# Optimization experiments

Hardware: AMD Instinct MI355X
Metric: run time of the kernel (lower is better)

## Reference

```python
import jax, jax.numpy as jnp
import numpy as np

B, T, C, H = 2, 2048, 2048, 16  # batch, seq_len, dim, num_heads
D = C // H  # head_dim = 128
ROPE_BASE = 10000.0


def apply_rope(x, pos):
    # x: [B, T, H, D]; adjacent-pair rotation (torchtune convention)
    d = x.shape[-1]
    inv_freq = 1.0 / (ROPE_BASE ** (jnp.arange(0, d, 2, dtype=jnp.float32) / d))  # [D/2]
    freqs = pos.astype(jnp.float32)[:, None] * inv_freq[None, :]                 # [T, D/2]
    cos = jnp.cos(freqs)[None, :, None, :]
    sin = jnp.sin(freqs)[None, :, None, :]
    x1 = x[..., 0::2]
    x2 = x[..., 1::2]
    out = jnp.stack([x1 * cos - x2 * sin, x2 * cos + x1 * sin], axis=-1)  # [B,T,H,D/2,2]
    return out.reshape(x.shape)


def setup_inputs() -> dict:
    key = jax.random.key(0)
    k1, k2, k3 = jax.random.split(key, 3)
    x = jax.random.normal(k1, (B, T, C), dtype=jnp.float32)
    # 0.02 init scale keeps attention logits in a sane range
    W_qkv = jax.random.normal(k2, (C, 3 * C), dtype=jnp.float32) * 0.02
    W_out = jax.random.normal(k3, (C, C), dtype=jnp.float32) * 0.02
    return {"x": x, "W_qkv": W_qkv, "W_out": W_out}


def reference(x, W_qkv, W_out):
    b, t, c = x.shape
    h, d = H, c // H
    # fused QKV projection
    qkv = (x @ W_qkv).reshape(b, t, 3, h, d)
    q, k, v = qkv[:, :, 0], qkv[:, :, 1], qkv[:, :, 2]  # [B,T,H,D] each
    pos = jnp.arange(t)  # cache_pos = 0 (prefill)
    q = apply_rope(q, pos)
    k = apply_rope(k, pos)
    scale = 1.0 / np.sqrt(d).astype(np.float32)
    scores = jnp.einsum('bqhd,bkhd->bhqk', q, k) * scale  # [B,H,T,T]
    causal = jnp.tril(jnp.ones((t, t), dtype=bool))
    scores = jnp.where(causal[None, None], scores, -jnp.inf)
    probs = jax.nn.softmax(scores, axis=-1)
    o = jnp.einsum('bhqk,bkhd->bqhd', probs, v).reshape(b, t, c)
    return o @ W_out
```

## Files before the change

kernel.cpp:

```cpp
#include <hip/hip_runtime.h>
#include <stdint.h>

#define TSEQ 2048

typedef __bf16 bf16x8 __attribute__((ext_vector_type(8)));
typedef float f32x4 __attribute__((ext_vector_type(4)));

typedef const __attribute__((address_space(1))) unsigned int* gas_u32;
typedef __attribute__((address_space(3))) unsigned int* las_u32;

__device__ __forceinline__ f32x4 mfma16(bf16x8 a, bf16x8 b, f32x4 c) {
  return __builtin_amdgcn_mfma_f32_16x16x32_bf16(a, b, c, 0, 0, 0);
}

__device__ __forceinline__ unsigned short f2b(float f) {
  unsigned int u = __float_as_uint(f);
  u += 0x7fffu + ((u >> 16) & 1u);
  return (unsigned short)(u >> 16);
}

__device__ __forceinline__ void gload_lds16(const unsigned short* g, unsigned short* l) {
  __builtin_amdgcn_global_load_lds((gas_u32)(const void*)g, (las_u32)(void*)l, 16, 0, 0);
}

__global__ __launch_bounds__(256) void cast_bf16_kernel(const float* __restrict__ src,
                                                        unsigned short* __restrict__ dst) {
  size_t i = ((size_t)blockIdx.x * 256 + threadIdx.x) * 4;
  float4 v = *(const float4*)(src + i);
  ushort4 o;
  o.x = f2b(v.x); o.y = f2b(v.y); o.z = f2b(v.z); o.w = f2b(v.w);
  *(ushort4*)(dst + i) = o;
}

__device__ __forceinline__ void transpose_tile(const float* __restrict__ src,
                                               unsigned short* __restrict__ dst,
                                               int R, int Cc, int cb, int rb) {
  __shared__ float tile[64][65];
  int t = threadIdx.x;
  int tr = t >> 4;
  int tc = (t & 15) * 4;
#pragma unroll
  for (int i = 0; i < 4; i++) {
    int r = tr + 16 * i;
    float4 v = *(const float4*)(src + (size_t)(rb + r) * Cc + cb + tc);
    tile[r][tc + 0] = v.x; tile[r][tc + 1] = v.y;
    tile[r][tc + 2] = v.z; tile[r][tc + 3] = v.w;
  }
  __syncthreads();
#pragma unroll
  for (int i = 0; i < 4; i++) {
    int r2 = tr + 16 * i;
    ushort4 o;
    o.x = f2b(tile[tc + 0][r2]);
    o.y = f2b(tile[tc + 1][r2]);
    o.z = f2b(tile[tc + 2][r2]);
    o.w = f2b(tile[tc + 3][r2]);
    *(ushort4*)(dst + (size_t)(cb + r2) * R + rb + tc) = o;
  }
}

__global__ __launch_bounds__(256) void transpose_cast2_kernel(const float* __restrict__ srcA,
                                                              unsigned short* __restrict__ dstA,
                                                              const float* __restrict__ srcB,
                                                              unsigned short* __restrict__ dstB) {
  int bx = blockIdx.x, rb = blockIdx.y * 64;
  if (bx < 96) transpose_tile(srcA, dstA, 2048, 6144, bx * 64, rb);
  else         transpose_tile(srcB, dstB, 2048, 2048, (bx - 96) * 64, rb);
}

__device__ __forceinline__ void gemm_core_256(const unsigned short* __restrict__ A,
                                              const unsigned short* __restrict__ Bt,
                                              int K, int bm, int bn,
                                              unsigned short* sm,
                                              f32x4 (&acc)[4][8]) {
  const int t = threadIdx.x;
  const int lane = t & 63, w = t >> 6;
  const int wloc = w & 3;
  const int wm = (wloc >> 1) * 64;
  const int wn = (wloc & 1) * 128;
  const int ks = w >> 2;
  const int quad = lane >> 4, l16 = lane & 15;
  const int rsw = l16 & 7;
  const int ch = ((ks * 4 + quad) ^ rsw) * 8;

  const int srow = t >> 3;
  const int gch = (t & 7) ^ (srow & 7);
  const unsigned short* pA = A + (size_t)(bm + srow) * K + gch * 8;
  const unsigned short* pB = Bt + (size_t)(bn + srow) * K + gch * 8;
  const size_t K64 = (size_t)64 * K;

  auto stageA = [&](int k0, unsigned short* dstSlot) {
    gload_lds16(pA + k0, dstSlot + t * 8);
    gload_lds16(pA + K64 + k0, dstSlot + (t + 512) * 8);
  };
  auto stageB01 = [&](int k0, unsigned short* dstSlot) {
    unsigned short* tB = dstSlot + 8192;
    gload_lds16(pB + k0, tB + t * 8);
    gload_lds16(pB + K64 + k0, tB + (t + 512) * 8);
  };
  auto stageB23 = [&](int k0, unsigned short* dstSlot) {
    unsigned short* tB = dstSlot + 8192;
    gload_lds16(pB + 2 * K64 + k0, tB + (t + 1024) * 8);
    gload_lds16(pB + 3 * K64 + k0, tB + (t + 1536) * 8);
  };

  stageA(0, sm);          stageB01(0, sm);          stageB23(0, sm);
  stageA(64, sm + 24576); stageB01(64, sm + 24576); stageB23(64, sm + 24576);

  const int nIter = K >> 6;
  int scur = 0, sstg = 2;

#pragma unroll 1
  for (int it = 0; it < nIter; it++) {
    if (it + 1 < nIter)
      asm volatile("s_waitcnt vmcnt(6) lgkmcnt(0)" ::: "memory");
    else
      asm volatile("s_waitcnt vmcnt(0) lgkmcnt(0)" ::: "memory");
    __builtin_amdgcn_s_barrier();
    asm volatile("" ::: "memory");

    const unsigned short* sA = sm + scur * 24576;
    const unsigned short* sB = sA + 8192;
    unsigned short* tgt = sm + sstg * 24576;
    const bool doStage = (it + 2 < nIter);
    const int k2 = (it + 2) << 6;

    bf16x8 aF[4], bF[8];

    auto mm = [&](int jb) {
      __builtin_amdgcn_s_setprio(1);
#pragma unroll
      for (int i = 0; i < 4; i++)
#pragma unroll
        for (int j2 = 0; j2 < 2; j2++)
          acc[i][jb + j2] = mfma16(aF[i], bF[jb + j2], acc[i][jb + j2]);
      __builtin_amdgcn_s_setprio(0);
    };

#pragma unroll
    for (int i = 0; i < 4; i++)
      aF[i] = *(const bf16x8*)(sA + (wm + i * 16 + l16) * 64 + ch);
#pragma unroll
    for (int j = 0; j < 2; j++)
      bF[j] = *(const bf16x8*)(sB + (wn + j * 16 + l16) * 64 + ch);
    if (doStage) stageA(k2, tgt);
    mm(0);
#pragma unroll
    for (int j = 2; j < 4; j++)
      bF[j] = *(const bf16x8*)(sB + (wn + j * 16 + l16) * 64 + ch);
    if (doStage) stageB01(k2, tgt);
    mm(2);
#pragma unroll
    for (int j = 4; j < 6; j++)
      bF[j] = *(const bf16x8*)(sB + (wn + j * 16 + l16) * 64 + ch);
    if (doStage) stageB23(k2, tgt);
    mm(4);
#pragma unroll
    for (int j = 6; j < 8; j++)
      bF[j] = *(const bf16x8*)(sB + (wn + j * 16 + l16) * 64 + ch);
    mm(6);

    scur = (scur == 2) ? 0 : scur + 1;
    sstg = (sstg == 2) ? 0 : sstg + 1;
  }
  __syncthreads();

  {
    float* mbuf = (float*)sm;
    float* wb = mbuf + w * 4096;
    const int lane4 = lane * 4;
    if (w < 4) {
#pragma unroll
      for (int i2 = 0; i2 < 2; i2++)
#pragma unroll
        for (int j = 0; j < 8; j++)
          *(f32x4*)(wb + (i2 * 8 + j) * 256 + lane4) = acc[2 + i2][j];
    } else {
#pragma unroll
      for (int i2 = 0; i2 < 2; i2++)
#pragma unroll
        for (int j = 0; j < 8; j++)
          *(f32x4*)(wb + (i2 * 8 + j) * 256 + lane4) = acc[i2][j];
    }
    __syncthreads();
    const float* pb = mbuf + (w ^ 4) * 4096;
    if (w < 4) {
#pragma unroll
      for (int i2 = 0; i2 < 2; i2++)
#pragma unroll
        for (int j = 0; j < 8; j++)
          acc[i2][j] += *(const f32x4*)(pb + (i2 * 8 + j) * 256 + lane4);
    } else {
#pragma unroll
      for (int i2 = 0; i2 < 2; i2++)
#pragma unroll
        for (int j = 0; j < 8; j++)
          acc[i2][j] = acc[2 + i2][j] + *(const f32x4*)(pb + (i2 * 8 + j) * 256 + lane4);
    }
  }
}

__global__ __launch_bounds__(512, 2) void gemm_qkv_rope(const unsigned short* __restrict__ Xb,
                                                        const unsigned short* __restrict__ Wqt,
                                                        unsigned short* __restrict__ Qd,
                                                        unsigned short* __restrict__ Kd,
                                                        unsigned short* __restrict__ Vtd) {
  __shared__ unsigned short smem[73728];
  f32x4 acc[4][8];
  const f32x4 z = {0.f, 0.f, 0.f, 0.f};
#pragma unroll
  for (int i = 0; i < 4; i++)
#pragma unroll
    for (int j = 0; j < 8; j++) acc[i][j] = z;

  const int bm = blockIdx.y * 128;
  const int bn = blockIdx.x * 256;
  gemm_core_256(Xb, Wqt, 2048, bm, bn, smem, acc);

  const int c0 = blockIdx.x * 2;
  const int s = c0 >> 4;
  const int hA = c0 & 15, hB = (c0 + 1) & 15;
  const int t = threadIdx.x, lane = t & 63, w = t >> 6;
  const int wloc = w & 3;
  const int wm = (wloc >> 1) * 64, wn = (wloc & 1) * 128;
  const int rowbase = wm + (w >> 2) * 32;
  const int quad = lane >> 4, l16 = lane & 15;
  const int bq = bm >> 11;
  const int tpos0 = bm & (TSEQ - 1);

  __syncthreads();
  unsigned short* sC = smem;

  if (s < 2) {
    const float scl = (s == 0) ? 0.08838834764831845f : 1.0f;
#pragma unroll
    for (int j = 0; j < 8; j++) {
      int d = wn + j * 16 + l16;
      int dh = d & 127;
      float invf = __expf(-(float)(dh >> 1) * 0.14391157f);
#pragma unroll
      for (int i = 0; i < 2; i++) {
#pragma unroll
        for (int r = 0; r < 4; r++) {
          int row = rowbase + i * 16 + quad * 4 + r;
          float ang = (float)(tpos0 + row) * invf;
          float sn, cs;
          __sincosf(ang, &sn, &cs);
          float v = acc[i][j][r];
          float p = __shfl_xor(v, 1, 64);
          float outv = (d & 1) ? (v * cs + p * sn) : (v * cs - p * sn);
          sC[row * 264 + d] = f2b(outv * scl);
        }
      }
    }
    __syncthreads();
    unsigned short* dst = (s == 0) ? Qd : Kd;
#pragma unroll
    for (int it = 0; it < 8; it++) {
      int u = t + 512 * it;
      int row = u >> 5, cc = u & 31;
      int hl = cc >> 4;
      size_t gb = ((size_t)(bq * 16 + (hl ? hB : hA)) * TSEQ + tpos0 + row) * 128 + (cc & 15) * 8;
      *(uint4*)(dst + gb) = *(const uint4*)(sC + row * 264 + cc * 8);
    }
  } else {
#pragma unroll
    for (int j = 0; j < 8; j++) {
      int d = wn + j * 16 + l16;
#pragma unroll
      for (int i = 0; i < 2; i++)
#pragma unroll
        for (int r = 0; r < 4; r++) {
          int col = rowbase + i * 16 + quad * 4 + r;
          sC[d * 136 + col] = f2b(acc[i][j][r]);
        }
    }
    __syncthreads();
#pragma unroll
    for (int it = 0; it < 8; it++) {
      int u = t + 512 * it;
      int dd = u >> 4, cc = u & 15;
      int hl = dd >> 7, dl = dd & 127;
      size_t gb = ((size_t)(bq * 16 + (hl ? hB : hA)) * 128 + dl) * TSEQ + tpos0 + cc * 8;
      *(uint4*)(Vtd + gb) = *(const uint4*)(sC + dd * 136 + cc * 8);
    }
  }
}

__global__ __launch_bounds__(256, 2) void attn_kernel(const unsigned short* __restrict__ Q,
                                                      const unsigned short* __restrict__ Kmat,
                                                      const unsigned short* __restrict__ Vt,
                                                      unsigned short* __restrict__ Ob) {
  __shared__ unsigned short smem[37376];
  const int pair = blockIdx.x, bh = blockIdx.y;
  const int qA = pair, qB = 31 - pair;
  const int t = threadIdx.x, lane = t & 63, w = t >> 6, quad = lane >> 4, l16 = lane & 15;
  const size_t base = (size_t)bh * TSEQ * 128;
  const unsigned short* Qp = Q + base;
  const unsigned short* Kp = Kmat + base;
  const unsigned short* Vp = Vt + base;
  unsigned short* myP = smem + 32768 + w * 1152;

  bf16x8 aqA[4], aqB[4];
  {
    int qrA = qA * 64 + w * 16 + l16;
    int qrB = qB * 64 + w * 16 + l16;
#pragma unroll
    for (int kk = 0; kk < 4; kk++) {
      aqA[kk] = *(const bf16x8*)(Qp + (size_t)qrA * 128 + kk * 32 + quad * 8);
      aqB[kk] = *(const bf16x8*)(Qp + (size_t)qrB * 128 + kk * 32 + quad * 8);
    }
  }
  const f32x4 z = {0.f, 0.f, 0.f, 0.f};
  f32x4 oA[8], oB[8];
  float mA[4], lA[4], mB[4], lB[4];
#pragma unroll
  for (int dt = 0; dt < 8; dt++) { oA[dt] = z; oB[dt] = z; }
#pragma unroll
  for (int r = 0; r < 4; r++) { mA[r] = -1e30f; lA[r] = 0.f; mB[r] = -1e30f; lB[r] = 0.f; }

  auto load_tiles = [&](int kb, int buf) {
    unsigned short* bK = smem + buf * 16384;
    unsigned short* bV = bK + 8192;
    const unsigned short* Kt = Kp + (size_t)kb * 64 * 128;
#pragma unroll
    for (int i2 = 0; i2 < 4; i2++) {
      int idx = t + 256 * i2;
      int r = idx >> 4, cS = idx & 15;
      int c = cS ^ (r & 7);
      gload_lds16(Kt + r * 128 + c * 8, bK + idx * 8);
    }
#pragma unroll
    for (int i2 = 0; i2 < 4; i2++) {
      int idx = t + 256 * i2;
      int r = idx >> 3, cS = idx & 7;
      int c = cS ^ (r & 7);
      gload_lds16(Vp + (size_t)r * TSEQ + kb * 64 + c * 8, bV + idx * 8);
    }
  };

  auto process = [&](bf16x8 (&aq)[4], f32x4 (&o)[8], float (&mst)[4], float (&lst)[4],
                     int qb, int kb, const unsigned short* bK, const unsigned short* bV) {
    f32x4 S[4];
#pragma unroll
    for (int nt = 0; nt < 4; nt++) {
      f32x4 sacc = z;
#pragma unroll
      for (int kk = 0; kk < 4; kk++) {
        const unsigned short* p =
            bK + (nt * 16 + l16) * 128 + (((kk * 4 + quad) ^ (l16 & 7)) * 8);
        sacc = mfma16(aq[kk], *(const bf16x8*)p, sacc);
      }
      S[nt] = sacc;
    }
    if (kb == qb) {
      int qg = qb * 64 + w * 16 + quad * 4;
#pragma unroll
      for (int nt = 0; nt < 4; nt++) {
        int key = kb * 64 + nt * 16 + l16;
#pragma unroll
        for (int r = 0; r < 4; r++)
          if (key > qg + r) S[nt][r] = -1e30f;
      }
    }
    float alpha[4];
#pragma unroll
    for (int r = 0; r < 4; r++) {
      float mx = fmaxf(fmaxf(S[0][r], S[1][r]), fmaxf(S[2][r], S[3][r]));
      mx = fmaxf(mx, __shfl_xor(mx, 1, 64));
      mx = fmaxf(mx, __shfl_xor(mx, 2, 64));
      mx = fmaxf(mx, __shfl_xor(mx, 4, 64));
      mx = fmaxf(mx, __shfl_xor(mx, 8, 64));
      float mnew = fmaxf(mst[r], mx);
      alpha[r] = __expf(mst[r] - mnew);
      mst[r] = mnew;
    }
    float rs[4] = {0.f, 0.f, 0.f, 0.f};
#pragma unroll
    for (int nt = 0; nt < 4; nt++)
#pragma unroll
      for (int r = 0; r < 4; r++) {
        float p = __expf(S[nt][r] - mst[r]);
        S[nt][r] = p;
        rs[r] += p;
      }
#pragma unroll
    for (int r = 0; r < 4; r++) {
      float s4 = rs[r];
      s4 += __shfl_xor(s4, 1, 64);
      s4 += __shfl_xor(s4, 2, 64);
      s4 += __shfl_xor(s4, 4, 64);
      s4 += __shfl_xor(s4, 8, 64);
      lst[r] = lst[r] * alpha[r] + s4;
#pragma unroll
      for (int nt = 0; nt < 4; nt++)
        myP[(quad * 4 + r) * 72 + nt * 16 + l16] = f2b(S[nt][r]);
    }
#pragma unroll
    for (int dt = 0; dt < 8; dt++) {
      f32x4 ov = o[dt];
      ov[0] *= alpha[0]; ov[1] *= alpha[1]; ov[2] *= alpha[2]; ov[3] *= alpha[3];
      o[dt] = ov;
    }
#pragma unroll
    for (int kk = 0; kk < 2; kk++) {
      bf16x8 ap = *(const bf16x8*)(myP + l16 * 72 + kk * 32 + quad * 8);
#pragma unroll
      for (int dt = 0; dt < 8; dt++) {
        const unsigned short* p =
            bV + (dt * 16 + l16) * 64 + (((kk * 4 + quad) ^ (l16 & 7)) * 8);
        o[dt] = mfma16(ap, *(const bf16x8*)p, o[dt]);
      }
    }
  };

  load_tiles(0, 0);
#pragma unroll 1
  for (int kb = 0; kb <= qB; kb++) {
    __syncthreads();
    if (kb < qB) load_tiles(kb + 1, (kb + 1) & 1);
    const unsigned short* bK = smem + (kb & 1) * 16384;
    const unsigned short* bV = bK + 8192;
    process(aqB, oB, mB, lB, qB, kb, bK, bV);
    if (kb <= qA) process(aqA, oA, mA, lA, qA, kb, bK, bV);
  }

  __syncthreads();
  unsigned short* sOA = smem;
  unsigned short* sOB = smem + 8704;
#pragma unroll
  for (int dt = 0; dt < 8; dt++)
#pragma unroll
    for (int r = 0; r < 4; r++) {
      int row = w * 16 + quad * 4 + r;
      sOA[row * 136 + dt * 16 + l16] = f2b(oA[dt][r] / lA[r]);
      sOB[row * 136 + dt * 16 + l16] = f2b(oB[dt][r] / lB[r]);
    }
  __syncthreads();
  const int b = bh >> 4, h = bh & 15;
#pragma unroll
  for (int it = 0; it < 4; it++) {
    int c = t + 256 * it;
    int row = c >> 4, off = (c & 15) * 8;
    uint4 va = *(const uint4*)(sOA + row * 136 + off);
    *(uint4*)(Ob + (size_t)(b * TSEQ + qA * 64 + row) * 2048 + h * 128 + off) = va;
    uint4 vb = *(const uint4*)(sOB + row * 136 + off);
    *(uint4*)(Ob + (size_t)(b * TSEQ + qB * 64 + row) * 2048 + h * 128 + off) = vb;
  }
}

__global__ __launch_bounds__(512, 2) void gemm_out_kernel(const unsigned short* __restrict__ Ob,
                                                          const unsigned short* __restrict__ Wot,
                                                          float* __restrict__ Cout) {
  __shared__ unsigned short smem[73728];
  f32x4 acc[4][8];
  const f32x4 z = {0.f, 0.f, 0.f, 0.f};
#pragma unroll
  for (int i = 0; i < 4; i++)
#pragma unroll
    for (int j = 0; j < 8; j++) acc[i][j] = z;

  const int bm = blockIdx.y * 128, bn = blockIdx.x * 256;
  gemm_core_256(Ob, Wot, 2048, bm, bn, smem, acc);

  const int t = threadIdx.x, lane = t & 63, w = t >> 6;
  const int wloc = w & 3;
  const int wm = (wloc >> 1) * 64, wn = (wloc & 1) * 128;
  const int rowbase = wm + (w >> 2) * 32;
  const int quad = lane >> 4, l16 = lane & 15;
#pragma unroll
  for (int i = 0; i < 2; i++)
#pragma unroll
    for (int j = 0; j < 8; j++)
#pragma unroll
      for (int r = 0; r < 4; r++) {
        int row = bm + rowbase + i * 16 + quad * 4 + r;
        int col = bn + wn + j * 16 + l16;
        Cout[(size_t)row * 2048 + col] = acc[i][j][r];
      }
}

extern "C" void kernel_launch(void* const* d_in, const int* in_sizes, int n_in,
                              void* d_out, int out_size, void* d_ws, size_t ws_size,
                              hipStream_t stream) {
  (void)in_sizes; (void)n_in; (void)out_size; (void)ws_size;
  const float* x = (const float*)d_in[0];
  const float* Wqkv = (const float*)d_in[1];
  const float* Wout = (const float*)d_in[2];
  float* out = (float*)d_out;
  char* ws = (char*)d_ws;

  unsigned short* Xb  = (unsigned short*)(ws);
  unsigned short* Wqt = (unsigned short*)(ws + 16777216);
  unsigned short* Wot = (unsigned short*)(ws + 41943040);
  unsigned short* Qd  = (unsigned short*)(ws + 50331648);
  unsigned short* Kd  = (unsigned short*)(ws + 67108864);
  unsigned short* Vtd = (unsigned short*)(ws + 83886080);
  unsigned short* Obf = (unsigned short*)(ws + 100663296);

  cast_bf16_kernel<<<8192, 256, 0, stream>>>(x, Xb);
  transpose_cast2_kernel<<<dim3(128, 32), 256, 0, stream>>>(Wqkv, Wqt, Wout, Wot);
  gemm_qkv_rope<<<dim3(24, 32), 512, 0, stream>>>(Xb, Wqt, Qd, Kd, Vtd);
  attn_kernel<<<dim3(16, 32), 256, 0, stream>>>(Qd, Kd, Vtd, Obf);
  gemm_out_kernel<<<dim3(8, 32), 512, 0, stream>>>(Obf, Wot, out);
}
```

Measured before the change: 379.7 us.

## Share K/V LDS fragments across paired query tiles and merge prologue kernels

```diff
diff --git a/kernel.cpp b/kernel.cpp
--- a/kernel.cpp
+++ b/kernel.cpp
@@ -21,15 +21,6 @@
 
 __device__ __forceinline__ void gload_lds16(const unsigned short* g, unsigned short* l) {
   __builtin_amdgcn_global_load_lds((gas_u32)(const void*)g, (las_u32)(void*)l, 16, 0, 0);
-}
-
-__global__ __launch_bounds__(256) void cast_bf16_kernel(const float* __restrict__ src,
-                                                        unsigned short* __restrict__ dst) {
-  size_t i = ((size_t)blockIdx.x * 256 + threadIdx.x) * 4;
-  float4 v = *(const float4*)(src + i);
-  ushort4 o;
-  o.x = f2b(v.x); o.y = f2b(v.y); o.z = f2b(v.z); o.w = f2b(v.w);
-  *(ushort4*)(dst + i) = o;
 }
 
 __device__ __forceinline__ void transpose_tile(const float* __restrict__ src,
@@ -59,13 +50,25 @@
   }
 }
 
-__global__ __launch_bounds__(256) void transpose_cast2_kernel(const float* __restrict__ srcA,
-                                                              unsigned short* __restrict__ dstA,
-                                                              const float* __restrict__ srcB,
-                                                              unsigned short* __restrict__ dstB) {
-  int bx = blockIdx.x, rb = blockIdx.y * 64;
-  if (bx < 96) transpose_tile(srcA, dstA, 2048, 6144, bx * 64, rb);
-  else         transpose_tile(srcB, dstB, 2048, 2048, (bx - 96) * 64, rb);
+__global__ __launch_bounds__(256) void prologue_kernel(const float* __restrict__ x,
+                                                       unsigned short* __restrict__ Xb,
+                                                       const float* __restrict__ Wqkv,
+                                                       unsigned short* __restrict__ Wqt,
+                                                       const float* __restrict__ Wout,
+                                                       unsigned short* __restrict__ Wot) {
+  int n = blockIdx.x;
+  if (n < 8192) {
+    size_t i = ((size_t)n * 256 + threadIdx.x) * 4;
+    float4 v = *(const float4*)(x + i);
+    ushort4 o;
+    o.x = f2b(v.x); o.y = f2b(v.y); o.z = f2b(v.z); o.w = f2b(v.w);
+    *(ushort4*)(Xb + i) = o;
+  } else {
+    int m = n - 8192;
+    int bxx = m & 127, rb = (m >> 7) * 64;
+    if (bxx < 96) transpose_tile(Wqkv, Wqt, 2048, 6144, bxx * 64, rb);
+    else          transpose_tile(Wout, Wot, 2048, 2048, (bxx - 96) * 64, rb);
+  }
 }
 
 __device__ __forceinline__ void gemm_core_256(const unsigned short* __restrict__ A,
@@ -339,30 +342,8 @@
     }
   };
 
-  auto process = [&](bf16x8 (&aq)[4], f32x4 (&o)[8], float (&mst)[4], float (&lst)[4],
-                     int qb, int kb, const unsigned short* bK, const unsigned short* bV) {
-    f32x4 S[4];
-#pragma unroll
-    for (int nt = 0; nt < 4; nt++) {
-      f32x4 sacc = z;
-#pragma unroll
-      for (int kk = 0; kk < 4; kk++) {
-        const unsigned short* p =
-            bK + (nt * 16 + l16) * 128 + (((kk * 4 + quad) ^ (l16 & 7)) * 8);
-        sacc = mfma16(aq[kk], *(const bf16x8*)p, sacc);
-      }
-      S[nt] = sacc;
-    }
-    if (kb == qb) {
-      int qg = qb * 64 + w * 16 + quad * 4;
-#pragma unroll
-      for (int nt = 0; nt < 4; nt++) {
-        int key = kb * 64 + nt * 16 + l16;
-#pragma unroll
-        for (int r = 0; r < 4; r++)
-          if (key > qg + r) S[nt][r] = -1e30f;
-      }
-    }
+  auto softmax_pv = [&](f32x4 (&S)[4], f32x4 (&o)[8], float (&mst)[4], float (&lst)[4],
+                        const unsigned short* bV, bool loadV, bf16x8 (&vr)[16]) {
     float alpha[4];
 #pragma unroll
     for (int r = 0; r < 4; r++) {
@@ -407,10 +388,22 @@
       bf16x8 ap = *(const bf16x8*)(myP + l16 * 72 + kk * 32 + quad * 8);
 #pragma unroll
       for (int dt = 0; dt < 8; dt++) {
-        const unsigned short* p =
-            bV + (dt * 16 + l16) * 64 + (((kk * 4 + quad) ^ (l16 & 7)) * 8);
-        o[dt] = mfma16(ap, *(const bf16x8*)p, o[dt]);
+        if (loadV)
+          vr[kk * 8 + dt] = *(const bf16x8*)(bV + (dt * 16 + l16) * 64 +
+                                             (((kk * 4 + quad) ^ (l16 & 7)) * 8));
+        o[dt] = mfma16(ap, vr[kk * 8 + dt], o[dt]);
       }
+    }
+  };
+
+  auto mask_tile = [&](f32x4 (&S)[4], int qb, int kb) {
+    int qg = qb * 64 + w * 16 + quad * 4;
+#pragma unroll
+    for (int nt = 0; nt < 4; nt++) {
+      int key = kb * 64 + nt * 16 + l16;
+#pragma unroll
+      for (int r = 0; r < 4; r++)
+        if (key > qg + r) S[nt][r] = -1e30f;
     }
   };
 
@@ -421,8 +414,42 @@
     if (kb < qB) load_tiles(kb + 1, (kb + 1) & 1);
     const unsigned short* bK = smem + (kb & 1) * 16384;
     const unsigned short* bV = bK + 8192;
-    process(aqB, oB, mB, lB, qB, kb, bK, bV);
-    if (kb <= qA) process(aqA, oA, mA, lA, qA, kb, bK, bV);
+
+    if (kb <= qA) {
+      f32x4 SB[4], SA[4];
+#pragma unroll
+      for (int nt = 0; nt < 4; nt++) {
+        f32x4 sb = z, sa = z;
+#pragma unroll
+        for (int kk = 0; kk < 4; kk++) {
+          bf16x8 kf = *(const bf16x8*)(bK + (nt * 16 + l16) * 128 +
+                                       (((kk * 4 + quad) ^ (l16 & 7)) * 8));
+          sb = mfma16(aqB[kk], kf, sb);
+          sa = mfma16(aqA[kk], kf, sa);
+        }
+        SB[nt] = sb; SA[nt] = sa;
+      }
+      if (kb == qA) mask_tile(SA, qA, kb);
+      bf16x8 vr[16];
+      softmax_pv(SB, oB, mB, lB, bV, true, vr);
+      softmax_pv(SA, oA, mA, lA, bV, false, vr);
+    } else {
+      f32x4 SB[4];
+#pragma unroll
+      for (int nt = 0; nt < 4; nt++) {
+        f32x4 sb = z;
+#pragma unroll
+        for (int kk = 0; kk < 4; kk++) {
+          bf16x8 kf = *(const bf16x8*)(bK + (nt * 16 + l16) * 128 +
+                                       (((kk * 4 + quad) ^ (l16 & 7)) * 8));
+          sb = mfma16(aqB[kk], kf, sb);
+        }
+        SB[nt] = sb;
+      }
+      if (kb == qB) mask_tile(SB, qB, kb);
+      bf16x8 vr[16];
+      softmax_pv(SB, oB, mB, lB, bV, true, vr);
+    }
   }
 
   __syncthreads();
@@ -498,8 +525,7 @@
   unsigned short* Vtd = (unsigned short*)(ws + 83886080);
   unsigned short* Obf = (unsigned short*)(ws + 100663296);
 
-  cast_bf16_kernel<<<8192, 256, 0, stream>>>(x, Xb);
-  transpose_cast2_kernel<<<dim3(128, 32), 256, 0, stream>>>(Wqkv, Wqt, Wout, Wot);
+  prologue_kernel<<<12288, 256, 0, stream>>>(x, Xb, Wqkv, Wqt, Wout, Wot);
   gemm_qkv_rope<<<dim3(24, 32), 512, 0, stream>>>(Xb, Wqt, Qd, Kd, Vtd);
   attn_kernel<<<dim3(16, 32), 256, 0, stream>>>(Qd, Kd, Vtd, Obf);
   gemm_out_kernel<<<dim3(8, 32), 512, 0, stream>>>(Obf, Wot, out);
```

Result: slower. 439.2 us (+15.7%).

## Merge prologue cast/transpose kernels and add intra-iteration barriers to GEMM core

Applied to the files above, without the earlier changes.

```diff
diff --git a/kernel.cpp b/kernel.cpp
--- a/kernel.cpp
+++ b/kernel.cpp
@@ -21,15 +21,6 @@
 
 __device__ __forceinline__ void gload_lds16(const unsigned short* g, unsigned short* l) {
   __builtin_amdgcn_global_load_lds((gas_u32)(const void*)g, (las_u32)(void*)l, 16, 0, 0);
-}
-
-__global__ __launch_bounds__(256) void cast_bf16_kernel(const float* __restrict__ src,
-                                                        unsigned short* __restrict__ dst) {
-  size_t i = ((size_t)blockIdx.x * 256 + threadIdx.x) * 4;
-  float4 v = *(const float4*)(src + i);
-  ushort4 o;
-  o.x = f2b(v.x); o.y = f2b(v.y); o.z = f2b(v.z); o.w = f2b(v.w);
-  *(ushort4*)(dst + i) = o;
 }
 
 __device__ __forceinline__ void transpose_tile(const float* __restrict__ src,
@@ -59,13 +50,25 @@
   }
 }
 
-__global__ __launch_bounds__(256) void transpose_cast2_kernel(const float* __restrict__ srcA,
-                                                              unsigned short* __restrict__ dstA,
-                                                              const float* __restrict__ srcB,
-                                                              unsigned short* __restrict__ dstB) {
-  int bx = blockIdx.x, rb = blockIdx.y * 64;
-  if (bx < 96) transpose_tile(srcA, dstA, 2048, 6144, bx * 64, rb);
-  else         transpose_tile(srcB, dstB, 2048, 2048, (bx - 96) * 64, rb);
+__global__ __launch_bounds__(256) void prologue_kernel(const float* __restrict__ x,
+                                                       unsigned short* __restrict__ Xb,
+                                                       const float* __restrict__ Wqkv,
+                                                       unsigned short* __restrict__ Wqt,
+                                                       const float* __restrict__ Wout,
+                                                       unsigned short* __restrict__ Wot) {
+  int n = blockIdx.x;
+  if (n < 8192) {
+    size_t i = ((size_t)n * 256 + threadIdx.x) * 4;
+    float4 v = *(const float4*)(x + i);
+    ushort4 o;
+    o.x = f2b(v.x); o.y = f2b(v.y); o.z = f2b(v.z); o.w = f2b(v.w);
+    *(ushort4*)(Xb + i) = o;
+  } else {
+    int m = n - 8192;
+    int bxx = m & 127, rb = (m >> 7) * 64;
+    if (bxx < 96) transpose_tile(Wqkv, Wqt, 2048, 6144, bxx * 64, rb);
+    else          transpose_tile(Wout, Wot, 2048, 2048, (bxx - 96) * 64, rb);
+  }
 }
 
 __device__ __forceinline__ void gemm_core_256(const unsigned short* __restrict__ A,
@@ -117,7 +120,7 @@
     else
       asm volatile("s_waitcnt vmcnt(0) lgkmcnt(0)" ::: "memory");
     __builtin_amdgcn_s_barrier();
-    asm volatile("" ::: "memory");
+    __builtin_amdgcn_sched_barrier(0);
 
     const unsigned short* sA = sm + scur * 24576;
     const unsigned short* sB = sA + 8192;
@@ -136,6 +139,17 @@
           acc[i][jb + j2] = mfma16(aF[i], bF[jb + j2], acc[i][jb + j2]);
       __builtin_amdgcn_s_setprio(0);
     };
+    auto midbar = [&]() {
+      __builtin_amdgcn_sched_barrier(0);
+      __builtin_amdgcn_s_barrier();
+      asm volatile("s_waitcnt lgkmcnt(0)" ::: "memory");
+      __builtin_amdgcn_sched_barrier(0);
+    };
+    auto endbar = [&]() {
+      __builtin_amdgcn_sched_barrier(0);
+      __builtin_amdgcn_s_barrier();
+      __builtin_amdgcn_sched_barrier(0);
+    };
 
 #pragma unroll
     for (int i = 0; i < 4; i++)
@@ -144,21 +158,32 @@
     for (int j = 0; j < 2; j++)
       bF[j] = *(const bf16x8*)(sB + (wn + j * 16 + l16) * 64 + ch);
     if (doStage) stageA(k2, tgt);
+    midbar();
     mm(0);
+    endbar();
+
 #pragma unroll
     for (int j = 2; j < 4; j++)
       bF[j] = *(const bf16x8*)(sB + (wn + j * 16 + l16) * 64 + ch);
     if (doStage) stageB01(k2, tgt);
+    midbar();
     mm(2);
+    endbar();
+
 #pragma unroll
     for (int j = 4; j < 6; j++)
       bF[j] = *(const bf16x8*)(sB + (wn + j * 16 + l16) * 64 + ch);
     if (doStage) stageB23(k2, tgt);
+    midbar();
     mm(4);
+    endbar();
+
 #pragma unroll
     for (int j = 6; j < 8; j++)
       bF[j] = *(const bf16x8*)(sB + (wn + j * 16 + l16) * 64 + ch);
+    midbar();
     mm(6);
+    __builtin_amdgcn_sched_barrier(0);
 
     scur = (scur == 2) ? 0 : scur + 1;
     sstg = (sstg == 2) ? 0 : sstg + 1;
@@ -498,8 +523,7 @@
   unsigned short* Vtd = (unsigned short*)(ws + 83886080);
   unsigned short* Obf = (unsigned short*)(ws + 100663296);
 
-  cast_bf16_kernel<<<8192, 256, 0, stream>>>(x, Xb);
-  transpose_cast2_kernel<<<dim3(128, 32), 256, 0, stream>>>(Wqkv, Wqt, Wout, Wot);
+  prologue_kernel<<<12288, 256, 0, stream>>>(x, Xb, Wqkv, Wqt, Wout, Wot);
   gemm_qkv_rope<<<dim3(24, 32), 512, 0, stream>>>(Xb, Wqt, Qd, Kd, Vtd);
   attn_kernel<<<dim3(16, 32), 256, 0, stream>>>(Qd, Kd, Vtd, Obf);
   gemm_out_kernel<<<dim3(8, 32), 512, 0, stream>>>(Obf, Wot, out);
```

Measured after the change: 368.7 us. 2.9% less time.
